# Optimization experiments

Hardware: AMD Instinct MI355X
Metric: run time of the kernel (lower is better)

The kernel has to match this reference:

```python
import jax, jax.numpy as jnp
import numpy as np

B, S, D, H, BLEN, FF = 4, 4096, 1024, 16, 256, 4096
DH = D // H
NEG = -1e9
EPS = 1e-6


def setup_inputs() -> dict:
    key = jax.random.key(0)
    ks = jax.random.split(key, 8)
    s = 0.02
    return {
        "X": jax.random.normal(ks[0], (B, S, D), jnp.float32),
        "Wq": jax.random.normal(ks[1], (D, D), jnp.float32) * s,
        "Wk": jax.random.normal(ks[2], (D, D), jnp.float32) * s,
        "Wv": jax.random.normal(ks[3], (D, D), jnp.float32) * s,
        "Wo": jax.random.normal(ks[4], (D, D), jnp.float32) * s,
        "g_attn": jnp.ones((D,), jnp.float32),
        "b_attn": jnp.zeros((D,), jnp.float32),
        "W1": jax.random.normal(ks[5], (D, FF), jnp.float32) * s,
        "b1": jnp.zeros((FF,), jnp.float32),
        "W2": jax.random.normal(ks[6], (FF, D), jnp.float32) * s,
        "b2": jnp.zeros((D,), jnp.float32),
        "g_ffn": jnp.ones((D,), jnp.float32),
        "b_ffn": jnp.zeros((D,), jnp.float32),
    }


def _layernorm(x, g, b):
    mu = jnp.mean(x, axis=-1, keepdims=True)
    var = jnp.mean(jnp.square(x - mu), axis=-1, keepdims=True)
    return (x - mu) * jax.lax.rsqrt(var + EPS) * g + b


def _local_attn(X, Wq, Wk, Wv, Wo):
    def split_heads(y):  # [B,S,D] -> [B,H,S,DH]
        return y.reshape(B, S, H, DH).transpose(0, 2, 1, 3)

    q = split_heads(X @ Wq) * (DH ** -0.5)
    k = split_heads(X @ Wk)
    v = split_heads(X @ Wv)

    nb = S // BLEN  # S is a multiple of BLEN, so the torch pad is a no-op
    q = q.reshape(B, H, nb, BLEN, DH)
    k = k.reshape(B, H, nb, BLEN, DH)
    v = v.reshape(B, H, nb, BLEN, DH)

    # First block: plain causal attention within block 0.
    causal = NEG * jnp.triu(jnp.ones((BLEN, BLEN), jnp.float32), 1)
    logits0 = jnp.einsum('bhkd,bhqd->bhqk', k[:, :, 0], q[:, :, 0]) + causal
    out0 = jax.nn.softmax(logits0, axis=-1) @ v[:, :, 0]  # [B,H,BLEN,DH]

    # Tail blocks attend to [previous block, current block].
    local_k = jnp.concatenate([k[:, :, :-1], k[:, :, 1:]], axis=3)  # [B,H,nb-1,2B,DH]
    local_v = jnp.concatenate([v[:, :, :-1], v[:, :, 1:]], axis=3)
    tail_q = q[:, :, 1:]
    bias = NEG * jnp.triu(jnp.ones((BLEN, 2 * BLEN), jnp.float32), BLEN + 1)
    logits = jnp.einsum('bhnkd,bhnqd->bhnqk', local_k, tail_q) + bias
    tail = jnp.einsum('bhnqk,bhnkd->bhnqd', jax.nn.softmax(logits, axis=-1), local_v)
    tail = tail.reshape(B, H, S - BLEN, DH)

    res = jnp.concatenate([out0, tail], axis=2)       # [B,H,S,DH]
    res = res.transpose(0, 2, 1, 3).reshape(B, S, D)  # merge heads
    return res @ Wo


def reference(X, Wq, Wk, Wv, Wo, g_attn, b_attn, W1, b1, W2, b2, g_ffn, b_ffn):
    y = _local_attn(X, Wq, Wk, Wv, Wo)
    X = _layernorm(y + X, g_attn, b_attn)
    y = jax.nn.relu(X @ W1 + b1) @ W2 + b2
    X = _layernorm(y + X, g_ffn, b_ffn)
    return X
```

## Files before the change

kernel.cpp:

```cpp
#include <hip/hip_runtime.h>
#include <stdint.h>

#define B_    4
#define S_    4096
#define D_    1024
#define H_    16
#define DH_   64
#define BLEN_ 256
#define FF_   4096
#define M_    16384

typedef unsigned short u16;
typedef __attribute__((ext_vector_type(8))) short s8v;
typedef __attribute__((ext_vector_type(4))) short s4v;
typedef __attribute__((ext_vector_type(4))) float f4v;

#define MFMA32(A,B,C) __builtin_amdgcn_mfma_f32_16x16x32_bf16(A,B,C,0,0,0)
#define BAR() asm volatile("s_barrier" ::: "memory")

__device__ __forceinline__ f4v mfma16(s4v a, s4v b, f4v c) {
#if defined(__HIP_DEVICE_COMPILE__)
#if __has_builtin(__builtin_amdgcn_mfma_f32_16x16x16bf16_1k)
  return __builtin_amdgcn_mfma_f32_16x16x16bf16_1k(a, b, c, 0, 0, 0);
#elif __has_builtin(__builtin_amdgcn_mfma_f32_16x16x16_bf16_1k)
  return __builtin_amdgcn_mfma_f32_16x16x16_bf16_1k(a, b, c, 0, 0, 0);
#elif __has_builtin(__builtin_amdgcn_mfma_f32_16x16x16_bf16)
  return __builtin_amdgcn_mfma_f32_16x16x16_bf16(a, b, c, 0, 0, 0);
#else
  f4v d;
  asm volatile("v_mfma_f32_16x16x16_bf16 %0, %1, %2, %3"
               : "=v"(d) : "v"(a), "v"(b), "v"(c));
  return d;
#endif
#else
  (void)a; (void)b; return c;
#endif
}

__device__ __forceinline__ u16 f2b(float f) {
  union { float f; unsigned u; } v; v.f = f;
  unsigned r = v.u + 0x7fffu + ((v.u >> 16) & 1u);
  return (u16)(r >> 16);
}
__device__ __forceinline__ float b2f(u16 h) {
  union { unsigned u; float f; } v; v.u = ((unsigned)h) << 16; return v.f;
}

__device__ __forceinline__ void gld16(const void* gp, void* lp) {
  __builtin_amdgcn_global_load_lds(
      (const __attribute__((address_space(1))) void*)(uintptr_t)gp,
      (__attribute__((address_space(3))) void*)(uintptr_t)lp, 16, 0, 0);
}


__global__ __launch_bounds__(256) void k_castx(const float* __restrict__ in, u16* __restrict__ out) {
  long i = (long)blockIdx.x * 256 + threadIdx.x;
  float4 v = ((const float4*)in)[i];
  s4v o; o[0] = (short)f2b(v.x); o[1] = (short)f2b(v.y);
  o[2] = (short)f2b(v.z); o[3] = (short)f2b(v.w);
  *(s4v*)(out + i * 4) = o;
}

__global__ __launch_bounds__(256) void k_wt(const float* __restrict__ in, u16* __restrict__ out,
                                            int K, int N, float scale) {
  long i = (long)blockIdx.x * 256 + threadIdx.x;
  if (i >= (long)K * N) return;
  int k = (int)(i / N), n = (int)(i % N);
  out[(long)n * K + k] = f2b(in[i] * scale);
}

template<int EPI, int K>
__global__ __launch_bounds__(512, 2) void k_gemm256(
    const u16* __restrict__ A, const u16* __restrict__ Bt,
    const float* __restrict__ bias, const void* __restrict__ res,
    u16* __restrict__ out, int N) {
  __shared__ __align__(16) u16 sA[2][16384];
  __shared__ __align__(16) u16 sB[2][16384];
  const int t = threadIdx.x, lane = t & 63, w = t >> 6;
  const int wm = w >> 2, wn = w & 3;
  const int nwg = gridDim.x, cpx = nwg >> 3, orig = blockIdx.x;
  const int wg = (orig & 7) * cpx + (orig >> 3);
  const int mb = wg & 63, nb = wg >> 6;
  const int m0 = mb << 8, n0 = nb << 8;
  constexpr int NT = K >> 6;

  const int srow = lane >> 3;
  const int scol = ((lane & 7) ^ srow) << 3;
  const u16* gA = A + (size_t)(m0 + srow) * K + scol;
  const u16* gB = Bt + (size_t)(n0 + srow) * K + scol;

  auto stA = [&](int d, int h, int kt) {
#pragma unroll
    for (int i = 0; i < 2; i++) {
      int c = i * 8 + w;
      gld16(gA + (size_t)(h * 128 + c * 8) * K + kt * 64, &sA[d][h * 8192 + c * 512]);
    }
  };
  auto stB = [&](int d, int h, int kt) {
#pragma unroll
    for (int i = 0; i < 2; i++) {
      int c = i * 8 + w;
      gld16(gB + (size_t)(h * 128 + c * 8) * K + kt * 64, &sB[d][h * 8192 + c * 512]);
    }
  };

  const int swz = (lane & 7) << 4;
  const int g8b = (lane >> 4) << 4;
  const int r16 = lane & 15;
  auto rdA = [&](int d, int mt, int kh) -> s8v {
    int byt = (mt * 32 + wm * 16 + r16) * 128 + ((kh * 64 + g8b) ^ swz);
    return *(const s8v*)((const char*)sA[d] + byt);
  };
  auto rdB = [&](int d, int nt, int kh) -> s8v {
    int byt = (nt * 64 + wn * 16 + r16) * 128 + ((kh * 64 + g8b) ^ swz);
    return *(const s8v*)((const char*)sB[d] + byt);
  };

  f4v acc[8][4];
  f4v zz = {0.f, 0.f, 0.f, 0.f};
#pragma unroll
  for (int i = 0; i < 8; i++)
#pragma unroll
    for (int j = 0; j < 4; j++) acc[i][j] = zz;

  stA(0, 0, 0); stB(0, 0, 0); stA(0, 1, 0); stB(0, 1, 0);
  stA(1, 0, 1); stB(1, 0, 1);
  asm volatile("s_waitcnt vmcnt(4)" ::: "memory");
  BAR();

  s8v af[4][2], af2[4][2], b0[2][2], b1[2][2];
#pragma unroll
  for (int mt = 0; mt < 4; mt++) { af[mt][0] = rdA(0, mt, 0); af[mt][1] = rdA(0, mt, 1); }
#pragma unroll
  for (int nt = 0; nt < 2; nt++) { b0[nt][0] = rdB(0, nt, 0); b0[nt][1] = rdB(0, nt, 1); }

  for (int j = 0; j < NT; ++j) {
    const int d = j & 1, nd = d ^ 1;
    const bool s1 = (j + 1 < NT), s2 = (j + 2 < NT);

#pragma unroll
    for (int nt = 0; nt < 2; nt++) { b1[nt][0] = rdB(d, nt + 2, 0); b1[nt][1] = rdB(d, nt + 2, 1); }
    if (s1) stB(nd, 1, j + 1);
    __builtin_amdgcn_s_setprio(1);
#pragma unroll
    for (int mt = 0; mt < 4; mt++)
#pragma unroll
      for (int nt = 0; nt < 2; nt++) {
        acc[mt][nt] = MFMA32(af[mt][0], b0[nt][0], acc[mt][nt]);
        acc[mt][nt] = MFMA32(af[mt][1], b0[nt][1], acc[mt][nt]);
      }
    __builtin_amdgcn_s_setprio(0);

#pragma unroll
    for (int mt = 0; mt < 4; mt++) { af2[mt][0] = rdA(d, mt + 4, 0); af2[mt][1] = rdA(d, mt + 4, 1); }
    if (s1) stA(nd, 1, j + 1);
    __builtin_amdgcn_s_setprio(1);
#pragma unroll
    for (int mt = 0; mt < 4; mt++)
#pragma unroll
      for (int nt = 0; nt < 2; nt++) {
        acc[mt][nt + 2] = MFMA32(af[mt][0], b1[nt][0], acc[mt][nt + 2]);
        acc[mt][nt + 2] = MFMA32(af[mt][1], b1[nt][1], acc[mt][nt + 2]);
      }
    __builtin_amdgcn_s_setprio(0);
    BAR();

    if (s2) stA(d, 0, j + 2);
    __builtin_amdgcn_s_setprio(1);
#pragma unroll
    for (int mt = 0; mt < 4; mt++)
#pragma unroll
      for (int nt = 0; nt < 2; nt++) {
        acc[mt + 4][nt] = MFMA32(af2[mt][0], b0[nt][0], acc[mt + 4][nt]);
        acc[mt + 4][nt] = MFMA32(af2[mt][1], b0[nt][1], acc[mt + 4][nt]);
      }
    __builtin_amdgcn_s_setprio(0);
    BAR();

    if (s2) stB(d, 0, j + 2);
    __builtin_amdgcn_s_setprio(1);
#pragma unroll
    for (int mt = 0; mt < 4; mt++)
#pragma unroll
      for (int nt = 0; nt < 2; nt++) {
        acc[mt + 4][nt + 2] = MFMA32(af2[mt][0], b1[nt][0], acc[mt + 4][nt + 2]);
        acc[mt + 4][nt + 2] = MFMA32(af2[mt][1], b1[nt][1], acc[mt + 4][nt + 2]);
      }
    __builtin_amdgcn_s_setprio(0);
    if (s2) asm volatile("s_waitcnt vmcnt(4)" ::: "memory");
    else    asm volatile("s_waitcnt vmcnt(0)" ::: "memory");
    BAR();
    if (s1) {
#pragma unroll
      for (int mt = 0; mt < 4; mt++) { af[mt][0] = rdA(nd, mt, 0); af[mt][1] = rdA(nd, mt, 1); }
#pragma unroll
      for (int nt = 0; nt < 2; nt++) { b0[nt][0] = rdB(nd, nt, 0); b0[nt][1] = rdB(nd, nt, 1); }
    }
  }

  const int g4 = (lane >> 4) << 2;
#pragma unroll
  for (int mt = 0; mt < 8; mt++) {
#pragma unroll
    for (int nt = 0; nt < 4; nt++) {
      const int col = n0 + nt * 64 + wn * 16 + r16;
      const long rbase = m0 + mt * 32 + wm * 16 + g4;
      float bcol = 0.f;
      if constexpr (EPI == 2 || EPI == 3) bcol = bias[col];
#pragma unroll
      for (int r = 0; r < 4; r++) {
        long idx = (rbase + r) * (long)N + col;
        float v = acc[mt][nt][r];
        if constexpr (EPI == 1) v += ((const float*)res)[idx];
        if constexpr (EPI == 2) { v += bcol; v = fmaxf(v, 0.f); }
        if constexpr (EPI == 3) { v += bcol + b2f(((const u16*)res)[idx]); }
        out[idx] = f2b(v);
      }
    }
  }
}

__global__ __launch_bounds__(256) void k_attn(const u16* __restrict__ QKV, u16* __restrict__ Aout) {
  __shared__ __align__(16) u16 sK[64 * 64];
  __shared__ __align__(16) u16 sVT[64 * 64];
  const int t = threadIdx.x, lane = t & 63, w = t >> 6;
  const int qblock = blockIdx.x;
  const int b = blockIdx.y >> 4, h = blockIdx.y & 15;
  const int qcol = lane & 15, g = lane >> 4, g4 = g << 2;
  const int win = (qblock == 0) ? 0 : (qblock - 1) * BLEN_;
  const int nch = (qblock == 0) ? 4 : 8;
  const int qbw = qblock * BLEN_ + w * 64;
  const long rowbase = (long)b * S_;
  const int LDQ = 3072;

  s8v qf[4][2];
#pragma unroll
  for (int nt = 0; nt < 4; nt++)
#pragma unroll
    for (int kh = 0; kh < 2; kh++)
      qf[nt][kh] = *(const s8v*)(QKV + (rowbase + qbw + nt * 16 + qcol) * LDQ + h * DH_ + kh * 32 + (g << 3));

  f4v zz = {0.f, 0.f, 0.f, 0.f};
  f4v acc[4][4];
#pragma unroll
  for (int i = 0; i < 4; i++)
#pragma unroll
    for (int j = 0; j < 4; j++) acc[i][j] = zz;
  float mrow[4] = {-1e30f, -1e30f, -1e30f, -1e30f};
  float lrow[4] = {0.f, 0.f, 0.f, 0.f};

  for (int c = 0; c < nch; ++c) {
    const int kb = win + c * 64;
    __syncthreads();
#pragma unroll
    for (int p = 0; p < 2; p++) {
      int key = p * 32 + (t >> 3);
      int d8 = (t & 7) << 3;
      s8v kv = *(const s8v*)(QKV + (rowbase + kb + key) * LDQ + 1024 + h * DH_ + d8);
      int bo = key * 128 + d8 * 2; bo ^= (key & 7) << 4;
      *(s8v*)((char*)sK + bo) = kv;
    }
#pragma unroll
    for (int p = 0; p < 2; p++) {
      int key = (t & 31) + (p << 5);
      int d8 = (t >> 5) << 3;
      s8v vv = *(const s8v*)(QKV + (rowbase + kb + key) * LDQ + 2048 + h * DH_ + d8);
#pragma unroll
      for (int j = 0; j < 8; j++) {
        int dh = d8 + j;
        int bo = dh * 128 + key * 2; bo ^= (dh & 7) << 3;
        *(u16*)((char*)sVT + bo) = (u16)vv[j];
      }
    }
    __syncthreads();
    if (kb > qbw + 63) continue;

    f4v st[4][4];
#pragma unroll
    for (int i = 0; i < 4; i++)
#pragma unroll
      for (int j = 0; j < 4; j++) st[i][j] = zz;
#pragma unroll
    for (int kh = 0; kh < 2; kh++) {
#pragma unroll
      for (int mt = 0; mt < 4; mt++) {
        int key = mt * 16 + qcol;
        int bo = key * 128 + kh * 64 + (g << 4); bo ^= (key & 7) << 4;
        s8v kf = *(const s8v*)((const char*)sK + bo);
#pragma unroll
        for (int nt = 0; nt < 4; nt++) st[mt][nt] = MFMA32(kf, qf[nt][kh], st[mt][nt]);
      }
    }
    if (kb + 63 > qbw) {
#pragma unroll
      for (int mt = 0; mt < 4; mt++) {
        int kbase = kb + mt * 16 + g4;
#pragma unroll
        for (int nt = 0; nt < 4; nt++) {
          int qabs = qbw + nt * 16 + qcol;
#pragma unroll
          for (int r = 0; r < 4; r++)
            if (kbase + r > qabs) st[mt][nt][r] = -1e30f;
        }
      }
    }
    s4v pf[4][4];
#pragma unroll
    for (int nt = 0; nt < 4; nt++) {
      float cm = -1e30f;
#pragma unroll
      for (int mt = 0; mt < 4; mt++)
#pragma unroll
        for (int r = 0; r < 4; r++) cm = fmaxf(cm, st[mt][nt][r]);
      cm = fmaxf(cm, __shfl_xor(cm, 16));
      cm = fmaxf(cm, __shfl_xor(cm, 32));
      float mnew = fmaxf(mrow[nt], cm);
      float sc = __expf(mrow[nt] - mnew);
      mrow[nt] = mnew;
      float ps = 0.f;
#pragma unroll
      for (int kt = 0; kt < 4; kt++) {
        s4v pp;
#pragma unroll
        for (int r = 0; r < 4; r++) {
          float sv = st[kt][nt][r];
          float p = (sv > -1e29f) ? __expf(sv - mnew) : 0.f;
          ps += p;
          pp[r] = (short)f2b(p);
        }
        pf[nt][kt] = pp;
      }
      ps += __shfl_xor(ps, 16);
      ps += __shfl_xor(ps, 32);
      lrow[nt] = lrow[nt] * sc + ps;
#pragma unroll
      for (int dt = 0; dt < 4; dt++) acc[dt][nt] *= sc;
    }
#pragma unroll
    for (int dt = 0; dt < 4; dt++) {
      int dh = dt * 16 + qcol;
#pragma unroll
      for (int kt = 0; kt < 4; kt++) {
        int bo = dh * 128 + kt * 32 + (g << 3); bo ^= (dh & 7) << 3;
        s4v vf = *(const s4v*)((const char*)sVT + bo);
#pragma unroll
        for (int nt = 0; nt < 4; nt++) acc[dt][nt] = mfma16(vf, pf[nt][kt], acc[dt][nt]);
      }
    }
  }

#pragma unroll
  for (int nt = 0; nt < 4; nt++) {
    float inv = 1.f / lrow[nt];
    long qrow = rowbase + qbw + nt * 16 + qcol;
#pragma unroll
    for (int dt = 0; dt < 4; dt++) {
      s4v o;
#pragma unroll
      for (int r = 0; r < 4; r++) o[r] = (short)f2b(acc[dt][nt][r] * inv);
      *(s4v*)(Aout + qrow * D_ + h * DH_ + dt * 16 + g4) = o;
    }
  }
}

template<int OUTB>
__global__ __launch_bounds__(256) void k_ln(const u16* __restrict__ in, const float* __restrict__ gw,
                                            const float* __restrict__ bw, float* __restrict__ outf,
                                            u16* __restrict__ outb) {
  const int t = threadIdx.x, lane = t & 63, w = t >> 6;
  const long base = (long)blockIdx.x * D_;
  s4v xv = *(const s4v*)(in + base + t * 4);
  float v0 = b2f((u16)xv[0]), v1 = b2f((u16)xv[1]), v2 = b2f((u16)xv[2]), v3 = b2f((u16)xv[3]);
  float s = v0 + v1 + v2 + v3;
  float s2 = v0 * v0 + v1 * v1 + v2 * v2 + v3 * v3;
#pragma unroll
  for (int off = 1; off < 64; off <<= 1) { s += __shfl_xor(s, off); s2 += __shfl_xor(s2, off); }
  __shared__ float red[8];
  if (lane == 0) { red[w] = s; red[4 + w] = s2; }
  __syncthreads();
  s = red[0] + red[1] + red[2] + red[3];
  s2 = red[4] + red[5] + red[6] + red[7];
  float mu = s * (1.f / D_);
  float var = s2 * (1.f / D_) - mu * mu;
  float rstd = rsqrtf(var + 1e-6f);
  float4 gv = ((const float4*)gw)[t];
  float4 bv = ((const float4*)bw)[t];
  float o0 = (v0 - mu) * rstd * gv.x + bv.x;
  float o1 = (v1 - mu) * rstd * gv.y + bv.y;
  float o2 = (v2 - mu) * rstd * gv.z + bv.z;
  float o3 = (v3 - mu) * rstd * gv.w + bv.w;
  if constexpr (OUTB) {
    s4v o; o[0] = (short)f2b(o0); o[1] = (short)f2b(o1); o[2] = (short)f2b(o2); o[3] = (short)f2b(o3);
    *(s4v*)(outb + base + t * 4) = o;
  } else {
    float4 o; o.x = o0; o.y = o1; o.z = o2; o.w = o3;
    *(float4*)(outf + base + t * 4) = o;
  }
}


extern "C" void kernel_launch(void* const* d_in, const int* in_sizes, int n_in,
                              void* d_out, int out_size, void* d_ws, size_t ws_size,
                              hipStream_t stream) {
  const float* X      = (const float*)d_in[0];
  const float* Wq     = (const float*)d_in[1];
  const float* Wk     = (const float*)d_in[2];
  const float* Wv     = (const float*)d_in[3];
  const float* Wo     = (const float*)d_in[4];
  const float* g_attn = (const float*)d_in[5];
  const float* b_attn = (const float*)d_in[6];
  const float* W1     = (const float*)d_in[7];
  const float* b1     = (const float*)d_in[8];
  const float* W2     = (const float*)d_in[9];
  const float* b2     = (const float*)d_in[10];
  const float* g_ffn  = (const float*)d_in[11];
  const float* b_ffn  = (const float*)d_in[12];
  float* out = (float*)d_out;

  char* ws = (char*)d_ws;
  const size_t MB = 1ull << 20;
  u16* WqkvT = (u16*)(ws + 0 * MB);
  u16* WoT   = (u16*)(ws + 6 * MB);
  u16* W1T   = (u16*)(ws + 8 * MB);
  u16* W2T   = (u16*)(ws + 16 * MB);
  u16* Xb    = (u16*)(ws + 24 * MB);
  u16* QKVb  = (u16*)(ws + 56 * MB);
  u16* Ab    = (u16*)(ws + 152 * MB);
  u16* Yb    = (u16*)(ws + 184 * MB);
  u16* Mid   = QKVb;

  dim3 b256(256), b512(512);
  k_wt<<<dim3(4096),  b256, 0, stream>>>(Wq, WqkvT,                1024, 1024, 0.125f);
  k_wt<<<dim3(4096),  b256, 0, stream>>>(Wk, WqkvT + 1024 * 1024,  1024, 1024, 1.0f);
  k_wt<<<dim3(4096),  b256, 0, stream>>>(Wv, WqkvT + 2048 * 1024,  1024, 1024, 1.0f);
  k_wt<<<dim3(4096),  b256, 0, stream>>>(Wo, WoT, 1024, 1024, 1.0f);
  k_wt<<<dim3(16384), b256, 0, stream>>>(W1, W1T, 1024, 4096, 1.0f);
  k_wt<<<dim3(16384), b256, 0, stream>>>(W2, W2T, 4096, 1024, 1.0f);
  k_castx<<<dim3(16384), b256, 0, stream>>>(X, Xb);

  k_gemm256<0, 1024><<<dim3(768), b512, 0, stream>>>(Xb, WqkvT, nullptr, nullptr, QKVb, 3072);
  k_attn<<<dim3(16, B_ * H_), b256, 0, stream>>>(QKVb, Ab);
  k_gemm256<1, 1024><<<dim3(256), b512, 0, stream>>>(Ab, WoT, nullptr, X, Yb, 1024);
  k_ln<1><<<dim3(16384), b256, 0, stream>>>(Yb, g_attn, b_attn, nullptr, Xb);
  k_gemm256<2, 1024><<<dim3(1024), b512, 0, stream>>>(Xb, W1T, b1, nullptr, Mid, 4096);
  k_gemm256<3, 4096><<<dim3(256), b512, 0, stream>>>(Mid, W2T, b2, Xb, Yb, 1024);
  k_ln<0><<<dim3(16384), b256, 0, stream>>>(Yb, g_ffn, b_ffn, out, nullptr);

  (void)in_sizes; (void)n_in; (void)out_size; (void)ws_size;
}
```

Measured before the change: 661.5 us.

## Restructure GEMM mainloop into eight-phase pipeline and tile the weight transpose

The GEMM main loop becomes a fully unrolled sequence of eight phases per k-tile pair. Each phase issues LDS fragment reads and one global-to-LDS stage, waits on barriers and lgkmcnt, then runs a quadrant of MFMAs gated by explicit vmcnt counts. This keeps more loads in flight and spaces the loads more evenly across the MFMA work. Separately, the weight transpose/cast kernel now uses a 32x32 shared-memory tile so both its reads and writes are coalesced. The tighter vmcnt accounting and the extra barriers add risk of stalls or subtle ordering errors.

```diff
diff --git a/kernel.cpp b/kernel.cpp
--- a/kernel.cpp
+++ b/kernel.cpp
@@ -63,11 +63,50 @@
 
 __global__ __launch_bounds__(256) void k_wt(const float* __restrict__ in, u16* __restrict__ out,
                                             int K, int N, float scale) {
-  long i = (long)blockIdx.x * 256 + threadIdx.x;
-  if (i >= (long)K * N) return;
-  int k = (int)(i / N), n = (int)(i % N);
-  out[(long)n * K + k] = f2b(in[i] * scale);
-}
+  __shared__ u16 tile[32][33];
+  const int tx = threadIdx.x & 31, ty = threadIdx.x >> 5;
+  const int kb = blockIdx.y << 5, nb = blockIdx.x << 5;
+#pragma unroll
+  for (int r = 0; r < 4; r++) {
+    int row = ty + r * 8;
+    tile[row][tx] = f2b(in[(long)(kb + row) * N + nb + tx] * scale);
+  }
+  __syncthreads();
+#pragma unroll
+  for (int r = 0; r < 4; r++) {
+    int row = ty + r * 8;
+    out[(long)(nb + row) * K + kb + tx] = tile[tx][row];
+  }
+}
+
+template<int QM, int QN>
+__device__ __forceinline__ void phmfma(f4v (&acc)[8][4], s8v (&A)[4][2], s8v (&B)[2][2]) {
+#pragma unroll
+  for (int mt = 0; mt < 4; mt++)
+#pragma unroll
+    for (int nt = 0; nt < 2; nt++) {
+      acc[QM * 4 + mt][QN * 2 + nt] = MFMA32(A[mt][0], B[nt][0], acc[QM * 4 + mt][QN * 2 + nt]);
+      acc[QM * 4 + mt][QN * 2 + nt] = MFMA32(A[mt][1], B[nt][1], acc[QM * 4 + mt][QN * 2 + nt]);
+    }
+}
+
+#define RD_A(d, half, DST) \
+  _Pragma("unroll") for (int mt = 0; mt < 4; mt++) { \
+    DST[mt][0] = rdA(d, mt + (half) * 4, 0); DST[mt][1] = rdA(d, mt + (half) * 4, 1); }
+#define RD_B(d, half, DST) \
+  _Pragma("unroll") for (int nt = 0; nt < 2; nt++) { \
+    DST[nt][0] = rdB(d, nt + (half) * 2, 0); DST[nt][1] = rdB(d, nt + (half) * 2, 1); }
+
+#define PHASE(GATE, READS, STAGE, QM, QN, AA, BB) \
+  READS STAGE \
+  BAR(); \
+  asm volatile("s_waitcnt lgkmcnt(0)" ::: "memory"); \
+  __builtin_amdgcn_sched_barrier(0); \
+  __builtin_amdgcn_s_setprio(1); \
+  phmfma<QM, QN>(acc, AA, BB); \
+  __builtin_amdgcn_s_setprio(0); \
+  asm volatile("s_waitcnt vmcnt(" #GATE ")" ::: "memory"); \
+  BAR();
 
 template<int EPI, int K>
 __global__ __launch_bounds__(512, 2) void k_gemm256(
@@ -83,6 +122,7 @@
   const int mb = wg & 63, nb = wg >> 6;
   const int m0 = mb << 8, n0 = nb << 8;
   constexpr int NT = K >> 6;
+  constexpr int NP = NT >> 1;
 
   const int srow = lane >> 3;
   const int scol = ((lane & 7) ^ srow) << 3;
@@ -123,80 +163,32 @@
 #pragma unroll
     for (int j = 0; j < 4; j++) acc[i][j] = zz;
 
-  stA(0, 0, 0); stB(0, 0, 0); stA(0, 1, 0); stB(0, 1, 0);
-  stA(1, 0, 1); stB(1, 0, 1);
-  asm volatile("s_waitcnt vmcnt(4)" ::: "memory");
+  stA(0, 0, 0); stB(0, 0, 0); stB(0, 1, 0); stA(0, 1, 0);
+  stA(1, 0, 1); stB(1, 0, 1); stB(1, 1, 1);
+  asm volatile("s_waitcnt vmcnt(10)" ::: "memory");
   BAR();
 
-  s8v af[4][2], af2[4][2], b0[2][2], b1[2][2];
-#pragma unroll
-  for (int mt = 0; mt < 4; mt++) { af[mt][0] = rdA(0, mt, 0); af[mt][1] = rdA(0, mt, 1); }
-#pragma unroll
-  for (int nt = 0; nt < 2; nt++) { b0[nt][0] = rdB(0, nt, 0); b0[nt][1] = rdB(0, nt, 1); }
-
-  for (int j = 0; j < NT; ++j) {
-    const int d = j & 1, nd = d ^ 1;
-    const bool s1 = (j + 1 < NT), s2 = (j + 2 < NT);
-
-#pragma unroll
-    for (int nt = 0; nt < 2; nt++) { b1[nt][0] = rdB(d, nt + 2, 0); b1[nt][1] = rdB(d, nt + 2, 1); }
-    if (s1) stB(nd, 1, j + 1);
-    __builtin_amdgcn_s_setprio(1);
-#pragma unroll
-    for (int mt = 0; mt < 4; mt++)
-#pragma unroll
-      for (int nt = 0; nt < 2; nt++) {
-        acc[mt][nt] = MFMA32(af[mt][0], b0[nt][0], acc[mt][nt]);
-        acc[mt][nt] = MFMA32(af[mt][1], b0[nt][1], acc[mt][nt]);
-      }
-    __builtin_amdgcn_s_setprio(0);
-
-#pragma unroll
-    for (int mt = 0; mt < 4; mt++) { af2[mt][0] = rdA(d, mt + 4, 0); af2[mt][1] = rdA(d, mt + 4, 1); }
-    if (s1) stA(nd, 1, j + 1);
-    __builtin_amdgcn_s_setprio(1);
-#pragma unroll
-    for (int mt = 0; mt < 4; mt++)
-#pragma unroll
-      for (int nt = 0; nt < 2; nt++) {
-        acc[mt][nt + 2] = MFMA32(af[mt][0], b1[nt][0], acc[mt][nt + 2]);
-        acc[mt][nt + 2] = MFMA32(af[mt][1], b1[nt][1], acc[mt][nt + 2]);
-      }
-    __builtin_amdgcn_s_setprio(0);
-    BAR();
-
-    if (s2) stA(d, 0, j + 2);
-    __builtin_amdgcn_s_setprio(1);
-#pragma unroll
-    for (int mt = 0; mt < 4; mt++)
-#pragma unroll
-      for (int nt = 0; nt < 2; nt++) {
-        acc[mt + 4][nt] = MFMA32(af2[mt][0], b0[nt][0], acc[mt + 4][nt]);
-        acc[mt + 4][nt] = MFMA32(af2[mt][1], b0[nt][1], acc[mt + 4][nt]);
-      }
-    __builtin_amdgcn_s_setprio(0);
-    BAR();
-
-    if (s2) stB(d, 0, j + 2);
-    __builtin_amdgcn_s_setprio(1);
-#pragma unroll
-    for (int mt = 0; mt < 4; mt++)
-#pragma unroll
-      for (int nt = 0; nt < 2; nt++) {
-        acc[mt + 4][nt + 2] = MFMA32(af2[mt][0], b1[nt][0], acc[mt + 4][nt + 2]);
-        acc[mt + 4][nt + 2] = MFMA32(af2[mt][1], b1[nt][1], acc[mt + 4][nt + 2]);
-      }
-    __builtin_amdgcn_s_setprio(0);
-    if (s2) asm volatile("s_waitcnt vmcnt(4)" ::: "memory");
-    else    asm volatile("s_waitcnt vmcnt(0)" ::: "memory");
-    BAR();
-    if (s1) {
-#pragma unroll
-      for (int mt = 0; mt < 4; mt++) { af[mt][0] = rdA(nd, mt, 0); af[mt][1] = rdA(nd, mt, 1); }
-#pragma unroll
-      for (int nt = 0; nt < 2; nt++) { b0[nt][0] = rdB(nd, nt, 0); b0[nt][1] = rdB(nd, nt, 1); }
-    }
-  }
+  s8v a0[4][2], a1[4][2], bb0[2][2], bb1[2][2];
+
+  for (int pp = 0; pp < NP - 1; ++pp) {
+    const int j = pp * 2;
+    PHASE(10, RD_A(0, 0, a0) RD_B(0, 0, bb0), stA(1, 1, j + 1);, 0, 0, a0, bb0)
+    PHASE(10, RD_B(0, 1, bb1),                stA(0, 0, j + 2);, 0, 1, a0, bb1)
+    PHASE(10, RD_A(0, 1, a1),                 stB(0, 0, j + 2);, 1, 0, a1, bb0)
+    PHASE(10, ,                               stB(0, 1, j + 2);, 1, 1, a1, bb1)
+    PHASE(10, RD_A(1, 0, a0) RD_B(1, 0, bb0), stA(0, 1, j + 2);, 0, 0, a0, bb0)
+    PHASE(10, RD_B(1, 1, bb1),                stA(1, 0, j + 3);, 0, 1, a0, bb1)
+    PHASE(10, RD_A(1, 1, a1),                 stB(1, 0, j + 3);, 1, 0, a1, bb0)
+    PHASE(10, ,                               stB(1, 1, j + 3);, 1, 1, a1, bb1)
+  }
+  PHASE(10, RD_A(0, 0, a0) RD_B(0, 0, bb0), stA(1, 1, NT - 1);, 0, 0, a0, bb0)
+  PHASE(8,  RD_B(0, 1, bb1),                ,                   0, 1, a0, bb1)
+  PHASE(8,  RD_A(0, 1, a1),                 ,                   1, 0, a1, bb0)
+  PHASE(4,  ,                               ,                   1, 1, a1, bb1)
+  PHASE(2,  RD_A(1, 0, a0) RD_B(1, 0, bb0), ,                   0, 0, a0, bb0)
+  PHASE(0,  RD_B(1, 1, bb1),                ,                   0, 1, a0, bb1)
+  PHASE(0,  RD_A(1, 1, a1),                 ,                   1, 0, a1, bb0)
+  PHASE(0,  ,                               ,                   1, 1, a1, bb1)
 
   const int g4 = (lane >> 4) << 2;
 #pragma unroll
@@ -430,12 +422,12 @@
   u16* Mid   = QKVb;
 
   dim3 b256(256), b512(512);
-  k_wt<<<dim3(4096),  b256, 0, stream>>>(Wq, WqkvT,                1024, 1024, 0.125f);
-  k_wt<<<dim3(4096),  b256, 0, stream>>>(Wk, WqkvT + 1024 * 1024,  1024, 1024, 1.0f);
-  k_wt<<<dim3(4096),  b256, 0, stream>>>(Wv, WqkvT + 2048 * 1024,  1024, 1024, 1.0f);
-  k_wt<<<dim3(4096),  b256, 0, stream>>>(Wo, WoT, 1024, 1024, 1.0f);
-  k_wt<<<dim3(16384), b256, 0, stream>>>(W1, W1T, 1024, 4096, 1.0f);
-  k_wt<<<dim3(16384), b256, 0, stream>>>(W2, W2T, 4096, 1024, 1.0f);
+  k_wt<<<dim3(32, 32),  b256, 0, stream>>>(Wq, WqkvT,               1024, 1024, 0.125f);
+  k_wt<<<dim3(32, 32),  b256, 0, stream>>>(Wk, WqkvT + 1024 * 1024, 1024, 1024, 1.0f);
+  k_wt<<<dim3(32, 32),  b256, 0, stream>>>(Wv, WqkvT + 2048 * 1024, 1024, 1024, 1.0f);
+  k_wt<<<dim3(32, 32),  b256, 0, stream>>>(Wo, WoT, 1024, 1024, 1.0f);
+  k_wt<<<dim3(128, 32), b256, 0, stream>>>(W1, W1T, 1024, 4096, 1.0f);
+  k_wt<<<dim3(32, 128), b256, 0, stream>>>(W2, W2T, 4096, 1024, 1.0f);
   k_castx<<<dim3(16384), b256, 0, stream>>>(X, Xb);
 
   k_gemm256<0, 1024><<<dim3(768), b512, 0, stream>>>(Xb, WqkvT, nullptr, nullptr, QKVb, 3072);
```

Measured after the change: 602.4 us. 1.1x faster.
